# Kernel optimization log

Hardware: AMD Instinct MI355X
Metric: run time of the kernel (lower is better)

The kernel has to match this reference:

```python
import jax, jax.numpy as jnp
import numpy as np
from jax import lax

B, S, D = 2, 4096, 1024
E, H, K = 8, 2816, 2  # hidden_dim 4096 -> int(2*4096/3)=2730 -> round up to multiple_of 256 -> 2816


def setup_inputs() -> dict:
    key = jax.random.key(0)
    ks = jax.random.split(key, 5)
    scale = 0.02
    return {
        "x": jax.random.normal(ks[0], (B, S, D), dtype=jnp.float32),
        "router_w": jax.random.normal(ks[1], (E, D), dtype=jnp.float32) * scale,
        "w1": jax.random.normal(ks[2], (E, D, H), dtype=jnp.float32) * scale,
        "w2": jax.random.normal(ks[3], (E, H, D), dtype=jnp.float32) * scale,
        "w3": jax.random.normal(ks[4], (E, D, H), dtype=jnp.float32) * scale,
        "top_k": K,
    }


def reference(x, router_w, w1, w2, w3, top_k):
    b, s, d = x.shape
    e = router_w.shape[0]
    xf = x.reshape(-1, d)                                # [T, D]
    logits = xf @ router_w.T                             # [T, E]
    vals, idx = lax.top_k(logits, top_k)                 # [T, K]
    rw = jax.nn.softmax(vals.astype(jnp.float32), axis=-1).astype(x.dtype)  # [T, K]
    # combine[t, e] = routing weight of expert e for token t (0 if not selected)
    combine = jnp.sum(jax.nn.one_hot(idx, e, dtype=x.dtype) * rw[..., None], axis=1)  # [T, E]

    def body(acc, ew):
        w1e, w2e, w3e, ce = ew                           # [D,H], [H,D], [D,H], [T]
        h = jax.nn.silu(xf @ w1e) * (xf @ w3e)           # SwiGLU FFN, [T, H]
        return acc + (h @ w2e) * ce[:, None], None

    out, _ = lax.scan(body, jnp.zeros_like(xf), (w1, w2, w3, combine.T))
    return out.reshape(b, s, d)
```

## Files before the change

### kernel.cpp

```cpp
#include <hip/hip_runtime.h>
#include <stdint.h>

#define T_TOK 8192
#define DIM   1024
#define NE    8
#define NH    2816
#define NROWS (T_TOK*2)

typedef __attribute__((ext_vector_type(8))) __bf16 bf16x8;
typedef __attribute__((ext_vector_type(4))) float  f32x4;
typedef __attribute__((ext_vector_type(8))) unsigned short ushort8;

typedef __attribute__((address_space(1))) const unsigned int g_as1;
typedef __attribute__((address_space(3))) unsigned int l_as3;
#define GLL(g, l) __builtin_amdgcn_global_load_lds((g_as1*)(g), (l_as3*)(l), 16, 0, 0)
#define MFMA16(a,b,c) __builtin_amdgcn_mfma_f32_16x16x32_bf16(a,b,c,0,0,0)

__device__ __forceinline__ unsigned short f2bf(float f){
  union { float f; uint32_t u; } v; v.f = f;
  uint32_t r = (v.u + 0x7FFFu + ((v.u >> 16) & 1u)) >> 16;
  return (unsigned short)r;
}


__global__ void zero_init_k(float4* __restrict__ out, int* counts, int* cursor){
  if (blockIdx.x == 0 && threadIdx.x < NE){ counts[threadIdx.x] = 0; cursor[threadIdx.x] = 0; }
  int i = blockIdx.x*blockDim.x + threadIdx.x;
  const int n4 = T_TOK*DIM/4;
  const float4 z = make_float4(0.f,0.f,0.f,0.f);
  for (; i < n4; i += gridDim.x*blockDim.x) out[i] = z;
}

__global__ void cvt_k(const float* __restrict__ x, unsigned short* __restrict__ xbf){
  int i = blockIdx.x*blockDim.x + threadIdx.x;
  const int total = T_TOK*DIM/8;
  for (; i < total; i += gridDim.x*blockDim.x){
    const float4 a = *(const float4*)(x + (size_t)i*8);
    const float4 b = *(const float4*)(x + (size_t)i*8 + 4);
    ushort4 lo = make_ushort4(f2bf(a.x), f2bf(a.y), f2bf(a.z), f2bf(a.w));
    ushort4 hi = make_ushort4(f2bf(b.x), f2bf(b.y), f2bf(b.z), f2bf(b.w));
    *(ushort4*)(xbf + (size_t)i*8)     = lo;
    *(ushort4*)(xbf + (size_t)i*8 + 4) = hi;
  }
}


__global__ __launch_bounds__(256) void transpA_k(
    const float* __restrict__ w1, const float* __restrict__ w3,
    const float* __restrict__ w2,
    unsigned short* __restrict__ w1t, unsigned short* __restrict__ w3t,
    unsigned short* __restrict__ w2t, int zbase)
{
  __shared__ unsigned short Tl[64*72];
  const int z = zbase + blockIdx.y;
  const int f = blockIdx.x;
  const size_t DS = (size_t)DIM*NH;
  const float* src; unsigned short* dst; int R, C, rt, ct;
  if (z < 16){
    R = DIM; C = NH; rt = f/44; ct = f - rt*44;
    const int e = z & 7;
    src = (z < 8 ? w1 : w3) + (size_t)e*DS;
    dst = (z < 8 ? w1t : w3t) + (size_t)e*DS;
  } else {
    R = NH; C = DIM; rt = f/16; ct = f - rt*16;
    const int e = z - 16;
    src = w2 + (size_t)e*DS;
    dst = w2t + (size_t)e*DS;
  }
  const int r0 = rt*64, c0 = ct*64;
  const int t = threadIdx.x;
  #pragma unroll
  for (int i=0;i<4;i++){
    const int r  = (t>>4) + i*16;
    const int cq = t & 15;
    const float4 v = *(const float4*)(src + (size_t)(r0+r)*C + c0 + cq*4);
    Tl[(cq*4+0)*72 + r] = f2bf(v.x);
    Tl[(cq*4+1)*72 + r] = f2bf(v.y);
    Tl[(cq*4+2)*72 + r] = f2bf(v.z);
    Tl[(cq*4+3)*72 + r] = f2bf(v.w);
  }
  __syncthreads();
  #pragma unroll
  for (int i=0;i<2;i++){
    const int c  = i*32 + (t>>3);
    const int r8 = (t&7)*8;
    const ushort8 v = *(const ushort8*)&Tl[c*72 + r8];
    *(ushort8*)(dst + (size_t)(c0+c)*R + r0 + r8) = v;
  }
}


__global__ void router_k(const float* __restrict__ x, const float* __restrict__ rw,
                         unsigned short* __restrict__ xbf,
                         int* __restrict__ topk_e, float* __restrict__ topk_w,
                         int* __restrict__ counts){
  const int t = blockIdx.x;
  const int l = threadIdx.x;
  const float* xr = x + (size_t)t * DIM;
  unsigned short* xo = xbf + (size_t)t * DIM;
  float acc[NE];
  #pragma unroll
  for (int e=0;e<NE;e++) acc[e] = 0.f;
  #pragma unroll
  for (int i=0;i<4;i++){
    const int idx = l*4 + i*256;
    const float4 xv = *(const float4*)(xr + idx);
    ushort4 pk = make_ushort4(f2bf(xv.x), f2bf(xv.y), f2bf(xv.z), f2bf(xv.w));
    *(ushort4*)(xo + idx) = pk;
    #pragma unroll
    for (int e=0;e<NE;e++){
      const float4 wv = *(const float4*)(rw + e*DIM + idx);
      acc[e] += xv.x*wv.x + xv.y*wv.y + xv.z*wv.z + xv.w*wv.w;
    }
  }
  #pragma unroll
  for (int e=0;e<NE;e++){
    float v = acc[e];
    #pragma unroll
    for (int off=32; off; off>>=1) v += __shfl_xor(v, off);
    acc[e] = v;
  }
  if (l == 0){
    int e0 = 0; float v0 = acc[0];
    #pragma unroll
    for (int e=1;e<NE;e++) if (acc[e] > v0){ v0 = acc[e]; e0 = e; }
    int e1 = -1; float v1 = -1e30f;
    #pragma unroll
    for (int e=0;e<NE;e++) if (e != e0 && acc[e] > v1){ v1 = acc[e]; e1 = e; }
    float ex = __expf(v1 - v0);
    float s  = 1.f + ex;
    topk_e[t*2]   = e0;  topk_e[t*2+1] = e1;
    topk_w[t*2]   = 1.f/s; topk_w[t*2+1] = ex/s;
    atomicAdd(&counts[e0], 1);
    atomicAdd(&counts[e1], 1);
  }
}

__global__ void prefix_k(const int* __restrict__ counts, int* __restrict__ offs){
  if (threadIdx.x == 0 && blockIdx.x == 0){
    int s = 0;
    for (int e=0;e<NE;e++){ offs[e] = s; s += counts[e]; }
  }
}

__global__ void scatter_k(const int* __restrict__ topk_e, const float* __restrict__ topk_w,
                          const int* __restrict__ offs, int* __restrict__ cursor,
                          int* __restrict__ row_tok, float* __restrict__ row_w){
  int t = blockIdx.x*blockDim.x + threadIdx.x;
  if (t >= T_TOK) return;
  #pragma unroll
  for (int k=0;k<2;k++){
    int e = topk_e[t*2+k];
    int p = atomicAdd(&cursor[e], 1);
    int flat = offs[e] + p;
    row_tok[flat] = t;
    row_w[flat]   = topk_w[t*2+k];
  }
}


__global__ __launch_bounds__(512,2) void gemm1_p(
    const unsigned short* __restrict__ xbf,
    const unsigned short* __restrict__ w1t, const unsigned short* __restrict__ w3t,
    unsigned short* __restrict__ hbuf,
    const int* __restrict__ row_tok,
    const int* __restrict__ counts, const int* __restrict__ offs)
{
  __shared__ unsigned short As [3][128*32];
  __shared__ unsigned short B1s[3][128*32];
  __shared__ unsigned short B3s[3][128*32];

  const int i   = blockIdx.y*64 + blockIdx.x;
  const int lid = (i & 7)*1408 + (i >> 3);
  const int e   = lid / 1408;
  const int rem = lid - e*1408;
  const int h0  = (rem >> 6) * 128;
  const int rb  = rem & 63;

  const int cnt = counts[e];
  const int row0 = rb * 128;
  if (row0 >= cnt) return;
  const int nv   = min(128, cnt - row0);
  const int base = offs[e] + row0;
  const int NK   = DIM/32;

  const int t = threadIdx.x;
  const int r_loc = t >> 2, sct = t & 3;
  const int csw = (sct ^ ((r_loc >> 1) & 3)) * 8;
  const int tok = row_tok[base + min(r_loc, nv-1)];
  const unsigned short* aS  = xbf + (size_t)tok*DIM + csw;
  const unsigned short* b1S = w1t + ((size_t)(e*NH + h0) + r_loc)*DIM + csw;
  const unsigned short* b3S = w3t + ((size_t)(e*NH + h0) + r_loc)*DIM + csw;
  const int lo = t*16;

  const int wid = t >> 6, l = t & 63;
  const int wr = wid >> 2, wc = wid & 3;
  const int lr = l & 15,  lk = l >> 4;
  const int rc = (lk ^ ((lr >> 1) & 3)) * 8;

  f32x4 acc1[4][2], acc3[4][2];
  #pragma unroll
  for (int m=0;m<4;m++)
    #pragma unroll
    for (int n=0;n<2;n++){ acc1[m][n] = (f32x4)0.f; acc3[m][n] = (f32x4)0.f; }

  GLL(aS,    (char*)As[0]+lo); GLL(b1S,    (char*)B1s[0]+lo); GLL(b3S,    (char*)B3s[0]+lo);
  GLL(aS+32, (char*)As[1]+lo); GLL(b1S+32, (char*)B1s[1]+lo); GLL(b3S+32, (char*)B3s[1]+lo);

  for (int kt=0; kt<NK; ++kt){
    if (kt < NK-1) asm volatile("s_waitcnt vmcnt(3)" ::: "memory");
    else           asm volatile("s_waitcnt vmcnt(0)" ::: "memory");
    __builtin_amdgcn_s_barrier();

    if (kt+2 < NK){
      const int kA = (kt+2)*32;
      char* ad  = (char*)As [(kt+2)%3];
      char* b1d = (char*)B1s[(kt+2)%3];
      char* b3d = (char*)B3s[(kt+2)%3];
      GLL(aS+kA, ad+lo); GLL(b1S+kA, b1d+lo); GLL(b3S+kA, b3d+lo);
    }

    const unsigned short* Ab  = As [kt%3];
    const unsigned short* B1b = B1s[kt%3];
    const unsigned short* B3b = B3s[kt%3];

    bf16x8 a[4], b1[2], b3[2];
    #pragma unroll
    for (int m=0;m<4;m++) a[m] = *(const bf16x8*)&Ab[(wr*64 + m*16 + lr)*32 + rc];
    #pragma unroll
    for (int n=0;n<2;n++){
      b1[n] = *(const bf16x8*)&B1b[(wc*32 + n*16 + lr)*32 + rc];
      b3[n] = *(const bf16x8*)&B3b[(wc*32 + n*16 + lr)*32 + rc];
    }
    __builtin_amdgcn_s_setprio(1);
    #pragma unroll
    for (int m=0;m<4;m++)
      #pragma unroll
      for (int n=0;n<2;n++){
        acc1[m][n] = MFMA16(a[m], b1[n], acc1[m][n]);
        acc3[m][n] = MFMA16(a[m], b3[n], acc3[m][n]);
      }
    __builtin_amdgcn_s_setprio(0);
  }

  #pragma unroll
  for (int m=0;m<4;m++){
    #pragma unroll
    for (int i2=0;i2<4;i2++){
      const int r = wr*64 + m*16 + lk*4 + i2;
      if (r < nv){
        const size_t rowbase = (size_t)(base + r) * NH;
        #pragma unroll
        for (int n=0;n<2;n++){
          float z  = acc1[m][n][i2];
          float p3 = acc3[m][n][i2];
          float hv = (z / (1.f + __expf(-z))) * p3;
          hbuf[rowbase + h0 + wc*32 + n*16 + lr] = f2bf(hv);
        }
      }
    }
  }
}

__global__ __launch_bounds__(256,3) void gemm2_s(
    const unsigned short* __restrict__ hbuf,
    const unsigned short* __restrict__ w2t,
    float* __restrict__ out,
    const int* __restrict__ row_tok, const float* __restrict__ row_w,
    const int* __restrict__ counts, const int* __restrict__ offs)
{
  __shared__ unsigned short As[3][128*32];
  __shared__ unsigned short Bs[3][128*32];

  const int i   = blockIdx.y*64 + blockIdx.x;
  const int lid = (i & 7)*512 + (i >> 3);
  const int e   = lid >> 9;
  const int rem = lid & 511;
  const int d0  = (rem >> 6) * 128;
  const int rb  = rem & 63;

  const int cnt = counts[e];
  const int row0 = rb * 128;
  if (row0 >= cnt) return;
  const int nv   = min(128, cnt - row0);
  const int base = offs[e] + row0;
  const int NK   = NH/32;

  const int t = threadIdx.x;
  const int r_loc = t >> 2, sct = t & 3;
  const int csw = (sct ^ ((r_loc >> 1) & 3)) * 8;
  const unsigned short* aS0 = hbuf + (size_t)(base + min(r_loc,      nv-1))*NH + csw;
  const unsigned short* aS1 = hbuf + (size_t)(base + min(r_loc + 64, nv-1))*NH + csw;
  const unsigned short* bS0 = w2t + ((size_t)(e*DIM + d0) + r_loc)*NH + csw;
  const unsigned short* bS1 = bS0 + (size_t)64*NH;
  const int lo0 = t*16, lo1 = 4096 + t*16;

  const int wid = t >> 6, l = t & 63;
  const int wr = wid >> 1, wc = wid & 1;
  const int lr = l & 15,  lk = l >> 4;
  const int rc = (lk ^ ((lr >> 1) & 3)) * 8;

  f32x4 acc[4][4];
  #pragma unroll
  for (int m=0;m<4;m++)
    #pragma unroll
    for (int n=0;n<4;n++) acc[m][n] = (f32x4)0.f;

  GLL(aS0,    (char*)As[0]+lo0); GLL(aS1,    (char*)As[0]+lo1);
  GLL(bS0,    (char*)Bs[0]+lo0); GLL(bS1,    (char*)Bs[0]+lo1);
  GLL(aS0+32, (char*)As[1]+lo0); GLL(aS1+32, (char*)As[1]+lo1);
  GLL(bS0+32, (char*)Bs[1]+lo0); GLL(bS1+32, (char*)Bs[1]+lo1);

  for (int kt=0; kt<NK; ++kt){
    if (kt < NK-1) asm volatile("s_waitcnt vmcnt(4)" ::: "memory");
    else           asm volatile("s_waitcnt vmcnt(0)" ::: "memory");
    __builtin_amdgcn_s_barrier();

    if (kt+2 < NK){
      const int kA = (kt+2)*32;
      char* ad = (char*)As[(kt+2)%3];
      char* bd = (char*)Bs[(kt+2)%3];
      GLL(aS0+kA, ad+lo0); GLL(aS1+kA, ad+lo1);
      GLL(bS0+kA, bd+lo0); GLL(bS1+kA, bd+lo1);
    }

    const unsigned short* Ab = As[kt%3];
    const unsigned short* Bb = Bs[kt%3];

    bf16x8 a[4], b[4];
    #pragma unroll
    for (int m=0;m<4;m++) a[m] = *(const bf16x8*)&Ab[(wr*64 + m*16 + lr)*32 + rc];
    #pragma unroll
    for (int n=0;n<4;n++)  b[n] = *(const bf16x8*)&Bb[(wc*64 + n*16 + lr)*32 + rc];
    __builtin_amdgcn_s_setprio(1);
    #pragma unroll
    for (int m=0;m<4;m++)
      #pragma unroll
      for (int n=0;n<4;n++)
        acc[m][n] = MFMA16(a[m], b[n], acc[m][n]);
    __builtin_amdgcn_s_setprio(0);
  }

  #pragma unroll
  for (int m=0;m<4;m++){
    #pragma unroll
    for (int i2=0;i2<4;i2++){
      const int r = wr*64 + m*16 + lk*4 + i2;
      if (r < nv){
        const int flat = base + r;
        const int tok  = row_tok[flat];
        const float wgt = row_w[flat];
        float* orow = out + (size_t)tok * DIM + d0 + wc*64;
        #pragma unroll
        for (int n=0;n<4;n++)
          atomicAdd(&orow[n*16 + lr], acc[m][n][i2] * wgt);
      }
    }
  }
}


__global__ __launch_bounds__(256) void gemm1_k(
    const unsigned short* __restrict__ xbf,
    const float* __restrict__ w1, const float* __restrict__ w3,
    unsigned short* __restrict__ hbuf,
    const int* __restrict__ row_tok,
    const int* __restrict__ counts, const int* __restrict__ offs)
{
  __shared__ unsigned short Al [128*32];
  __shared__ unsigned short B1l[128*32];
  __shared__ unsigned short B3l[128*32];
  const int e   = blockIdx.y >> 6;
  const int rb  = blockIdx.y & 63;
  const int cnt = counts[e];
  const int row0 = rb * 128;
  if (row0 >= cnt) return;
  const int nv   = min(128, cnt - row0);
  const int base = offs[e] + row0;
  const int h0   = blockIdx.x * 128;
  const int t  = threadIdx.x;
  const int ar0 = t >> 2;
  const int ac  = t & 3;
  const int tok0 = row_tok[base + min(ar0,      nv-1)];
  const int tok1 = row_tok[base + min(ar0 + 64, nv-1)];
  const size_t asrc0 = (size_t)tok0 * DIM + ac*8;
  const size_t asrc1 = (size_t)tok1 * DIM + ac*8;
  const int dg = t >> 5;
  const int hq = t & 31;
  const float* w1p = w1 + (size_t)e * DIM * NH + (size_t)(h0 + hq*4);
  const float* w3p = w3 + (size_t)e * DIM * NH + (size_t)(h0 + hq*4);
  const int wid = t >> 6, l = t & 63;
  const int wr = wid >> 1, wc = wid & 1;
  const int lr = l & 15,  lk = l >> 4;
  f32x4 acc1[4][4], acc3[4][4];
  #pragma unroll
  for (int m=0;m<4;m++)
    #pragma unroll
    for (int n=0;n<4;n++){ acc1[m][n] = (f32x4)0.f; acc3[m][n] = (f32x4)0.f; }
  for (int kk=0; kk<DIM/32; ++kk){
    const int k0 = kk*32;
    __syncthreads();
    *(uint4*)&Al[ar0*32 + ac*8]      = *(const uint4*)(xbf + asrc0 + k0);
    *(uint4*)&Al[(ar0+64)*32 + ac*8] = *(const uint4*)(xbf + asrc1 + k0);
    {
      const float4 f0 = *(const float4*)(w1p + (size_t)(k0 + dg*4 + 0)*NH);
      const float4 f1 = *(const float4*)(w1p + (size_t)(k0 + dg*4 + 1)*NH);
      const float4 f2 = *(const float4*)(w1p + (size_t)(k0 + dg*4 + 2)*NH);
      const float4 f3 = *(const float4*)(w1p + (size_t)(k0 + dg*4 + 3)*NH);
      const float* p0=(const float*)&f0; const float* p1=(const float*)&f1;
      const float* p2=(const float*)&f2; const float* p3=(const float*)&f3;
      #pragma unroll
      for (int j=0;j<4;j++){
        ushort4 pk = make_ushort4(f2bf(p0[j]), f2bf(p1[j]), f2bf(p2[j]), f2bf(p3[j]));
        *(ushort4*)&B1l[(hq*4+j)*32 + dg*4] = pk;
      }
      const float4 g0 = *(const float4*)(w3p + (size_t)(k0 + dg*4 + 0)*NH);
      const float4 g1 = *(const float4*)(w3p + (size_t)(k0 + dg*4 + 1)*NH);
      const float4 g2 = *(const float4*)(w3p + (size_t)(k0 + dg*4 + 2)*NH);
      const float4 g3 = *(const float4*)(w3p + (size_t)(k0 + dg*4 + 3)*NH);
      const float* q0=(const float*)&g0; const float* q1=(const float*)&g1;
      const float* q2=(const float*)&g2; const float* q3=(const float*)&g3;
      #pragma unroll
      for (int j=0;j<4;j++){
        ushort4 pk = make_ushort4(f2bf(q0[j]), f2bf(q1[j]), f2bf(q2[j]), f2bf(q3[j]));
        *(ushort4*)&B3l[(hq*4+j)*32 + dg*4] = pk;
      }
    }
    __syncthreads();
    bf16x8 a[4], b1[4], b3[4];
    #pragma unroll
    for (int m=0;m<4;m++) a[m] = *(const bf16x8*)&Al[(wr*64 + m*16 + lr)*32 + lk*8];
    #pragma unroll
    for (int n=0;n<4;n++){
      b1[n] = *(const bf16x8*)&B1l[(wc*64 + n*16 + lr)*32 + lk*8];
      b3[n] = *(const bf16x8*)&B3l[(wc*64 + n*16 + lr)*32 + lk*8];
    }
    #pragma unroll
    for (int m=0;m<4;m++)
      #pragma unroll
      for (int n=0;n<4;n++){
        acc1[m][n] = MFMA16(a[m], b1[n], acc1[m][n]);
        acc3[m][n] = MFMA16(a[m], b3[n], acc3[m][n]);
      }
  }
  #pragma unroll
  for (int m=0;m<4;m++){
    #pragma unroll
    for (int i=0;i<4;i++){
      const int r = wr*64 + m*16 + lk*4 + i;
      if (r < nv){
        const size_t rowbase = (size_t)(base + r) * NH;
        #pragma unroll
        for (int n=0;n<4;n++){
          float z  = acc1[m][n][i];
          float p3 = acc3[m][n][i];
          float hv = (z / (1.f + __expf(-z))) * p3;
          hbuf[rowbase + h0 + wc*64 + n*16 + lr] = f2bf(hv);
        }
      }
    }
  }
}

__global__ __launch_bounds__(256) void gemm2_k(
    const unsigned short* __restrict__ hbuf,
    const float* __restrict__ w2,
    float* __restrict__ out,
    const int* __restrict__ row_tok, const float* __restrict__ row_w,
    const int* __restrict__ counts, const int* __restrict__ offs)
{
  __shared__ unsigned short Al[128*32];
  __shared__ unsigned short Bl[128*32];
  const int e   = blockIdx.y >> 6;
  const int rb  = blockIdx.y & 63;
  const int cnt = counts[e];
  const int row0 = rb * 128;
  if (row0 >= cnt) return;
  const int nv   = min(128, cnt - row0);
  const int base = offs[e] + row0;
  const int d0   = blockIdx.x * 128;
  const int t  = threadIdx.x;
  const int ar0 = t >> 2;
  const int ac  = t & 3;
  const size_t asrc0 = (size_t)(base + min(ar0,      nv-1)) * NH + ac*8;
  const size_t asrc1 = (size_t)(base + min(ar0 + 64, nv-1)) * NH + ac*8;
  const int dg = t >> 5;
  const int hq = t & 31;
  const float* w2p = w2 + (size_t)e * NH * DIM + (size_t)(d0 + hq*4);
  const int wid = t >> 6, l = t & 63;
  const int wr = wid >> 1, wc = wid & 1;
  const int lr = l & 15,  lk = l >> 4;
  f32x4 acc[4][4];
  #pragma unroll
  for (int m=0;m<4;m++)
    #pragma unroll
    for (int n=0;n<4;n++) acc[m][n] = (f32x4)0.f;
  for (int kk=0; kk<NH/32; ++kk){
    const int k0 = kk*32;
    __syncthreads();
    *(uint4*)&Al[ar0*32 + ac*8]      = *(const uint4*)(hbuf + asrc0 + k0);
    *(uint4*)&Al[(ar0+64)*32 + ac*8] = *(const uint4*)(hbuf + asrc1 + k0);
    {
      const float4 f0 = *(const float4*)(w2p + (size_t)(k0 + dg*4 + 0)*DIM);
      const float4 f1 = *(const float4*)(w2p + (size_t)(k0 + dg*4 + 1)*DIM);
      const float4 f2 = *(const float4*)(w2p + (size_t)(k0 + dg*4 + 2)*DIM);
      const float4 f3 = *(const float4*)(w2p + (size_t)(k0 + dg*4 + 3)*DIM);
      const float* p0=(const float*)&f0; const float* p1=(const float*)&f1;
      const float* p2=(const float*)&f2; const float* p3=(const float*)&f3;
      #pragma unroll
      for (int j=0;j<4;j++){
        ushort4 pk = make_ushort4(f2bf(p0[j]), f2bf(p1[j]), f2bf(p2[j]), f2bf(p3[j]));
        *(ushort4*)&Bl[(hq*4+j)*32 + dg*4] = pk;
      }
    }
    __syncthreads();
    bf16x8 a[4], b[4];
    #pragma unroll
    for (int m=0;m<4;m++) a[m] = *(const bf16x8*)&Al[(wr*64 + m*16 + lr)*32 + lk*8];
    #pragma unroll
    for (int n=0;n<4;n++)  b[n] = *(const bf16x8*)&Bl[(wc*64 + n*16 + lr)*32 + lk*8];
    #pragma unroll
    for (int m=0;m<4;m++)
      #pragma unroll
      for (int n=0;n<4;n++)
        acc[m][n] = MFMA16(a[m], b[n], acc[m][n]);
  }
  #pragma unroll
  for (int m=0;m<4;m++){
    #pragma unroll
    for (int i=0;i<4;i++){
      const int r = wr*64 + m*16 + lk*4 + i;
      if (r < nv){
        const int flat = base + r;
        const int tok  = row_tok[flat];
        const float wgt = row_w[flat];
        float* orow = out + (size_t)tok * DIM + d0 + wc*64;
        #pragma unroll
        for (int n=0;n<4;n++)
          atomicAdd(&orow[n*16 + lr], acc[m][n][i] * wgt);
      }
    }
  }
}


extern "C" void kernel_launch(void* const* d_in, const int* in_sizes, int n_in,
                              void* d_out, int out_size, void* d_ws, size_t ws_size,
                              hipStream_t stream) {
  (void)in_sizes; (void)n_in; (void)out_size;
  const float* x   = (const float*)d_in[0];
  const float* rw  = (const float*)d_in[1];
  const float* w1  = (const float*)d_in[2];
  const float* w2  = (const float*)d_in[3];
  const float* w3  = (const float*)d_in[4];
  float* out = (float*)d_out;
  char* ws = (char*)d_ws;

  const size_t SZ_XBF  = (size_t)T_TOK*DIM*2;
  const size_t SZ_HBUF = (size_t)NROWS*NH*2;
  const size_t SZ_WT   = (size_t)NE*NH*DIM*2;
  const size_t SZ_SMALL = (size_t)NROWS*4*2 + (size_t)T_TOK*2*4*2 + 3*64*4 + 4096;
  const size_t NEED_FAST = SZ_XBF + SZ_HBUF + 2*SZ_WT + SZ_SMALL;
  const size_t NEED_FULL = SZ_XBF + SZ_HBUF + 3*SZ_WT + SZ_SMALL;

  if (ws_size >= NEED_FAST) {
    const bool full = (ws_size >= NEED_FULL);
    size_t off = 0;
    unsigned short* xbf  = (unsigned short*)(ws + off); off += SZ_XBF;
    unsigned short* hbuf = (unsigned short*)(ws + off); off += SZ_HBUF;
    unsigned short* w1t  = (unsigned short*)(ws + off); off += SZ_WT;
    unsigned short* w3t  = (unsigned short*)(ws + off); off += SZ_WT;
    unsigned short* w2t;
    if (full){ w2t = (unsigned short*)(ws + off); off += SZ_WT; }
    else      { w2t = w1t; }
    int*   row_tok = (int*)  (ws + off); off += NROWS*4;
    float* row_w   = (float*)(ws + off); off += NROWS*4;
    int*   topk_e  = (int*)  (ws + off); off += T_TOK*2*4;
    float* topk_w  = (float*)(ws + off); off += T_TOK*2*4;
    int*   counts  = (int*)  (ws + off); off += 64;
    int*   offs    = (int*)  (ws + off); off += 64;
    int*   cursor  = (int*)  (ws + off); off += 64;

    zero_init_k<<<2048, 256, 0, stream>>>((float4*)out, counts, cursor);
    router_k   <<<T_TOK, 64, 0, stream>>>(x, rw, xbf, topk_e, topk_w, counts);
    prefix_k   <<<1, 64, 0, stream>>>(counts, offs);
    scatter_k  <<<(T_TOK+255)/256, 256, 0, stream>>>(topk_e, topk_w, offs, cursor, row_tok, row_w);
    if (full){
      transpA_k <<<dim3(704, 24), 256, 0, stream>>>(w1, w3, w2, w1t, w3t, w2t, 0);
      gemm1_p   <<<dim3(64, 176), 512, 0, stream>>>(xbf, w1t, w3t, hbuf, row_tok, counts, offs);
      gemm2_s   <<<dim3(64, NE*8), 256, 0, stream>>>(hbuf, w2t, out, row_tok, row_w, counts, offs);
    } else {
      transpA_k <<<dim3(704, 16), 256, 0, stream>>>(w1, w3, w2, w1t, w3t, w2t, 0);
      gemm1_p   <<<dim3(64, 176), 512, 0, stream>>>(xbf, w1t, w3t, hbuf, row_tok, counts, offs);
      transpA_k <<<dim3(704, 8), 256, 0, stream>>>(w1, w3, w2, w1t, w3t, w2t, 16);
      gemm2_s   <<<dim3(64, NE*8), 256, 0, stream>>>(hbuf, w2t, out, row_tok, row_w, counts, offs);
    }
  } else {
    size_t off = 0;
    unsigned short* xbf  = (unsigned short*)(ws + off); off += SZ_XBF;
    unsigned short* hbuf = (unsigned short*)(ws + off); off += SZ_HBUF;
    int*   row_tok = (int*)  (ws + off); off += NROWS*4;
    float* row_w   = (float*)(ws + off); off += NROWS*4;
    int*   topk_e  = (int*)  (ws + off); off += T_TOK*2*4;
    float* topk_w  = (float*)(ws + off); off += T_TOK*2*4;
    int*   counts  = (int*)  (ws + off); off += 64;
    int*   offs    = (int*)  (ws + off); off += 64;
    int*   cursor  = (int*)  (ws + off); off += 64;

    zero_init_k<<<2048, 256, 0, stream>>>((float4*)out, counts, cursor);
    router_k   <<<T_TOK, 64, 0, stream>>>(x, rw, xbf, topk_e, topk_w, counts);
    prefix_k   <<<1, 64, 0, stream>>>(counts, offs);
    scatter_k  <<<(T_TOK+255)/256, 256, 0, stream>>>(topk_e, topk_w, offs, cursor, row_tok, row_w);
    gemm1_k    <<<dim3(NH/128, NE*64), 256, 0, stream>>>(xbf, w1, w3, hbuf, row_tok, counts, offs);
    gemm2_k    <<<dim3(DIM/128, NE*64), 256, 0, stream>>>(hbuf, w2, out, row_tok, row_w, counts, offs);
  }
}
```

Before: 755.9 us.

## Replace atomic scatter-add in down-projection with per-row buffer and gather combine

The down-projection GEMM now writes each weighted expert row as bf16 into a per-assignment output buffer instead of doing fp32 atomicAdd into the token output. A new combine kernel sums each token's two rows into the output, which also removes the output zero-fill. Scatter records each assignment's flat position, and w2t is placed in the w3t slot and obuf in the w1t slot, so w2 is always transposed after gemm1. This removes atomic contention and zeroing traffic, at the cost of an extra bf16 round trip, an extra kernel and lower precision for the partial sums.

```diff
diff --git a/kernel.cpp b/kernel.cpp
--- a/kernel.cpp
+++ b/kernel.cpp
@@ -21,7 +21,16 @@
   uint32_t r = (v.u + 0x7FFFu + ((v.u >> 16) & 1u)) >> 16;
   return (unsigned short)r;
 }
-
+__device__ __forceinline__ float bf2f(unsigned short u){
+  union { uint32_t u; float f; } v; v.u = ((uint32_t)u) << 16;
+  return v.f;
+}
+
+
+__global__ void init2_k(int* counts, int* cursor){
+  int i = threadIdx.x;
+  if (i < NE){ counts[i] = 0; cursor[i] = 0; }
+}
 
 __global__ void zero_init_k(float4* __restrict__ out, int* counts, int* cursor){
   if (blockIdx.x == 0 && threadIdx.x < NE){ counts[threadIdx.x] = 0; cursor[threadIdx.x] = 0; }
@@ -29,19 +38,6 @@
   const int n4 = T_TOK*DIM/4;
   const float4 z = make_float4(0.f,0.f,0.f,0.f);
   for (; i < n4; i += gridDim.x*blockDim.x) out[i] = z;
-}
-
-__global__ void cvt_k(const float* __restrict__ x, unsigned short* __restrict__ xbf){
-  int i = blockIdx.x*blockDim.x + threadIdx.x;
-  const int total = T_TOK*DIM/8;
-  for (; i < total; i += gridDim.x*blockDim.x){
-    const float4 a = *(const float4*)(x + (size_t)i*8);
-    const float4 b = *(const float4*)(x + (size_t)i*8 + 4);
-    ushort4 lo = make_ushort4(f2bf(a.x), f2bf(a.y), f2bf(a.z), f2bf(a.w));
-    ushort4 hi = make_ushort4(f2bf(b.x), f2bf(b.y), f2bf(b.z), f2bf(b.w));
-    *(ushort4*)(xbf + (size_t)i*8)     = lo;
-    *(ushort4*)(xbf + (size_t)i*8 + 4) = hi;
-  }
 }
 
 
@@ -143,11 +139,15 @@
   }
 }
 
-__global__ void scatter_k(const int* __restrict__ topk_e, const float* __restrict__ topk_w,
-                          const int* __restrict__ offs, int* __restrict__ cursor,
-                          int* __restrict__ row_tok, float* __restrict__ row_w){
+__global__ void scatter2_k(const int* __restrict__ topk_e, const float* __restrict__ topk_w,
+                           const int* __restrict__ counts, int* __restrict__ cursor,
+                           int* __restrict__ row_tok, float* __restrict__ row_w,
+                           int* __restrict__ pos){
   int t = blockIdx.x*blockDim.x + threadIdx.x;
   if (t >= T_TOK) return;
+  int offs[NE]; int s = 0;
+  #pragma unroll
+  for (int e=0;e<NE;e++){ offs[e] = s; s += counts[e]; }
   #pragma unroll
   for (int k=0;k<2;k++){
     int e = topk_e[t*2+k];
@@ -155,7 +155,44 @@
     int flat = offs[e] + p;
     row_tok[flat] = t;
     row_w[flat]   = topk_w[t*2+k];
-  }
+    pos[t*2+k]    = flat;
+  }
+}
+
+__global__ void scatter_k(const int* __restrict__ topk_e, const float* __restrict__ topk_w,
+                          const int* __restrict__ offs, int* __restrict__ cursor,
+                          int* __restrict__ row_tok, float* __restrict__ row_w){
+  int t = blockIdx.x*blockDim.x + threadIdx.x;
+  if (t >= T_TOK) return;
+  #pragma unroll
+  for (int k=0;k<2;k++){
+    int e = topk_e[t*2+k];
+    int p = atomicAdd(&cursor[e], 1);
+    int flat = offs[e] + p;
+    row_tok[flat] = t;
+    row_w[flat]   = topk_w[t*2+k];
+  }
+}
+
+
+__global__ __launch_bounds__(256) void combine_k(
+    const unsigned short* __restrict__ obuf, const int* __restrict__ pos,
+    float* __restrict__ out)
+{
+  const int t = blockIdx.x;
+  const int p0 = pos[t*2], p1 = pos[t*2+1];
+  const unsigned short* r0 = obuf + (size_t)p0*DIM;
+  const unsigned short* r1 = obuf + (size_t)p1*DIM;
+  float* o = out + (size_t)t*DIM;
+  const int d = threadIdx.x*4;
+  const ushort4 a = *(const ushort4*)(r0 + d);
+  const ushort4 b = *(const ushort4*)(r1 + d);
+  float4 v;
+  v.x = bf2f(a.x) + bf2f(b.x);
+  v.y = bf2f(a.y) + bf2f(b.y);
+  v.z = bf2f(a.z) + bf2f(b.z);
+  v.w = bf2f(a.w) + bf2f(b.w);
+  *(float4*)(o + d) = v;
 }
 
 
@@ -262,11 +299,11 @@
   }
 }
 
-__global__ __launch_bounds__(256,3) void gemm2_s(
+__global__ __launch_bounds__(256,3) void gemm2_o(
     const unsigned short* __restrict__ hbuf,
     const unsigned short* __restrict__ w2t,
-    float* __restrict__ out,
-    const int* __restrict__ row_tok, const float* __restrict__ row_w,
+    unsigned short* __restrict__ obuf,
+    const float* __restrict__ row_w,
     const int* __restrict__ counts, const int* __restrict__ offs)
 {
   __shared__ unsigned short As[3][128*32];
@@ -348,12 +385,11 @@
       const int r = wr*64 + m*16 + lk*4 + i2;
       if (r < nv){
         const int flat = base + r;
-        const int tok  = row_tok[flat];
         const float wgt = row_w[flat];
-        float* orow = out + (size_t)tok * DIM + d0 + wc*64;
+        unsigned short* orow = obuf + (size_t)flat * DIM + d0 + wc*64;
         #pragma unroll
         for (int n=0;n<4;n++)
-          atomicAdd(&orow[n*16 + lr], acc[m][n][i2] * wgt);
+          orow[n*16 + lr] = f2bf(acc[m][n][i2] * wgt);
       }
     }
   }
@@ -559,42 +595,36 @@
   const size_t SZ_XBF  = (size_t)T_TOK*DIM*2;
   const size_t SZ_HBUF = (size_t)NROWS*NH*2;
   const size_t SZ_WT   = (size_t)NE*NH*DIM*2;
-  const size_t SZ_SMALL = (size_t)NROWS*4*2 + (size_t)T_TOK*2*4*2 + 3*64*4 + 4096;
+  const size_t SZ_OBUF = (size_t)NROWS*DIM*2;
+  const size_t SZ_SMALL = (size_t)NROWS*4*2 + (size_t)T_TOK*2*4*3 + 3*64*4 + 4096;
   const size_t NEED_FAST = SZ_XBF + SZ_HBUF + 2*SZ_WT + SZ_SMALL;
-  const size_t NEED_FULL = SZ_XBF + SZ_HBUF + 3*SZ_WT + SZ_SMALL;
 
   if (ws_size >= NEED_FAST) {
-    const bool full = (ws_size >= NEED_FULL);
     size_t off = 0;
     unsigned short* xbf  = (unsigned short*)(ws + off); off += SZ_XBF;
     unsigned short* hbuf = (unsigned short*)(ws + off); off += SZ_HBUF;
     unsigned short* w1t  = (unsigned short*)(ws + off); off += SZ_WT;
     unsigned short* w3t  = (unsigned short*)(ws + off); off += SZ_WT;
-    unsigned short* w2t;
-    if (full){ w2t = (unsigned short*)(ws + off); off += SZ_WT; }
-    else      { w2t = w1t; }
+    unsigned short* obuf = w1t;
+    unsigned short* w2t  = w3t;
     int*   row_tok = (int*)  (ws + off); off += NROWS*4;
     float* row_w   = (float*)(ws + off); off += NROWS*4;
     int*   topk_e  = (int*)  (ws + off); off += T_TOK*2*4;
     float* topk_w  = (float*)(ws + off); off += T_TOK*2*4;
+    int*   pos     = (int*)  (ws + off); off += T_TOK*2*4;
     int*   counts  = (int*)  (ws + off); off += 64;
     int*   offs    = (int*)  (ws + off); off += 64;
     int*   cursor  = (int*)  (ws + off); off += 64;
 
-    zero_init_k<<<2048, 256, 0, stream>>>((float4*)out, counts, cursor);
-    router_k   <<<T_TOK, 64, 0, stream>>>(x, rw, xbf, topk_e, topk_w, counts);
-    prefix_k   <<<1, 64, 0, stream>>>(counts, offs);
-    scatter_k  <<<(T_TOK+255)/256, 256, 0, stream>>>(topk_e, topk_w, offs, cursor, row_tok, row_w);
-    if (full){
-      transpA_k <<<dim3(704, 24), 256, 0, stream>>>(w1, w3, w2, w1t, w3t, w2t, 0);
-      gemm1_p   <<<dim3(64, 176), 512, 0, stream>>>(xbf, w1t, w3t, hbuf, row_tok, counts, offs);
-      gemm2_s   <<<dim3(64, NE*8), 256, 0, stream>>>(hbuf, w2t, out, row_tok, row_w, counts, offs);
-    } else {
-      transpA_k <<<dim3(704, 16), 256, 0, stream>>>(w1, w3, w2, w1t, w3t, w2t, 0);
-      gemm1_p   <<<dim3(64, 176), 512, 0, stream>>>(xbf, w1t, w3t, hbuf, row_tok, counts, offs);
-      transpA_k <<<dim3(704, 8), 256, 0, stream>>>(w1, w3, w2, w1t, w3t, w2t, 16);
-      gemm2_s   <<<dim3(64, NE*8), 256, 0, stream>>>(hbuf, w2t, out, row_tok, row_w, counts, offs);
-    }
+    init2_k   <<<1, 64, 0, stream>>>(counts, cursor);
+    router_k  <<<T_TOK, 64, 0, stream>>>(x, rw, xbf, topk_e, topk_w, counts);
+    prefix_k  <<<1, 64, 0, stream>>>(counts, offs);
+    scatter2_k<<<(T_TOK+255)/256, 256, 0, stream>>>(topk_e, topk_w, counts, cursor, row_tok, row_w, pos);
+    transpA_k <<<dim3(704, 16), 256, 0, stream>>>(w1, w3, w2, w1t, w3t, w2t, 0);
+    gemm1_p   <<<dim3(64, 176), 512, 0, stream>>>(xbf, w1t, w3t, hbuf, row_tok, counts, offs);
+    transpA_k <<<dim3(704, 8), 256, 0, stream>>>(w1, w3, w2, w1t, w3t, w2t, 16);
+    gemm2_o   <<<dim3(64, NE*8), 256, 0, stream>>>(hbuf, w2t, obuf, row_w, counts, offs);
+    combine_k <<<T_TOK, 256, 0, stream>>>(obuf, pos, out);
   } else {
     size_t off = 0;
     unsigned short* xbf  = (unsigned short*)(ws + off); off += SZ_XBF;
```

New measurement: 704.8 us. 6.8% less time.
